# Kernel optimization log

Measured on AMD Instinct MI355X. Metric: run time of the kernel, lower is better.

## Reference

```python
import jax, jax.numpy as jnp
import numpy as np

N, D_IN, UNITS = 8192, 4096, 4096

def setup_inputs() -> dict:
    key = jax.random.key(0)
    k1, k2 = jax.random.split(key)
    x = jax.random.normal(k1, (N, D_IN), dtype=jnp.float32)
    # weight initialized RandomNormal(stddev=0.1) in the original build()
    w = jax.random.normal(k2, (D_IN, UNITS), dtype=jnp.float32) * 0.1
    return {"x": x, "w": w}

def reference(x, w):
    # BinaryDense: sign-binarize both activations and weights, then dense matmul.
    # tf.sign semantics: sign(0) == 0, matched by jnp.sign.
    x_bin = jnp.sign(x)  # [N, d_in]
    w_bin = jnp.sign(w)  # [d_in, units]
    return jnp.matmul(x_bin, w_bin)  # [N, units]
```

## Files before the change

### kernel.cpp

```cpp
#include <hip/hip_runtime.h>
#include <stdint.h>

#define M_DIM 8192
#define K_DIM 4096
#define N_DIM 4096
#define KB (K_DIM / 2)

typedef unsigned char u8;
typedef unsigned int u32;
typedef int i32x4 __attribute__((ext_vector_type(4)));
typedef int i32x8 __attribute__((ext_vector_type(8)));
typedef float f32x4 __attribute__((ext_vector_type(4)));
typedef float float4v __attribute__((ext_vector_type(4)));
typedef u32 u32x2 __attribute__((ext_vector_type(2)));

__device__ __forceinline__ u32 sign_fp4(float v) {
  return v > 0.0f ? 0x2u : (v < 0.0f ? 0xAu : 0x0u);
}

__device__ __forceinline__ u32 pk16(u32 v) {
  return (v & 0xFu) | ((v >> 4) & 0xF0u) | ((v >> 8) & 0xF00u) | ((v >> 12) & 0xF000u);
}

__global__ void binarize_fused(const float* __restrict__ x, const float* __restrict__ w,
                               u32* __restrict__ xb, u8* __restrict__ wT) {
  const int tid = threadIdx.x;
  if (blockIdx.x < 4096) {
    __shared__ u8 tile[64][68];
    const int bid = blockIdx.x;
    const int bn = (bid & 63) * 64;
    const int bk = (bid >> 6) * 64;

#pragma unroll
    for (int it = 0; it < 4; ++it) {
      int idx = tid + it * 256;
      int r = idx >> 4;
      int c = (idx & 15) * 4;
      float4v v = *(const float4v*)&w[(size_t)(bk + r) * N_DIM + bn + c];
      tile[c + 0][r] = (u8)sign_fp4(v.x);
      tile[c + 1][r] = (u8)sign_fp4(v.y);
      tile[c + 2][r] = (u8)sign_fp4(v.z);
      tile[c + 3][r] = (u8)sign_fp4(v.w);
    }
    __syncthreads();
    const int rn = tid >> 2;
    const int cbyte = (tid & 3) * 8;
    const u32* trow = (const u32*)&tile[rn][0];
    u32 q0 = trow[cbyte / 2 + 0];
    u32 q1 = trow[cbyte / 2 + 1];
    u32 q2 = trow[cbyte / 2 + 2];
    u32 q3 = trow[cbyte / 2 + 3];
    u32x2 o;
    o.x = pk16(q0) | (pk16(q1) << 16);
    o.y = pk16(q2) | (pk16(q3) << 16);
    *(u32x2*)&wT[(size_t)(bn + rn) * KB + (bk >> 1) + cbyte] = o;
  } else {
    const int n8 = M_DIM * K_DIM / 8;
    int i = (blockIdx.x - 4096) * 256 + tid;
    const int stride = 2048 * 256;
    for (; i < n8; i += stride) {
      float4v v0 = ((const float4v*)x)[2 * i];
      float4v v1 = ((const float4v*)x)[2 * i + 1];
      u32 wd = sign_fp4(v0.x) | (sign_fp4(v0.y) << 4) | (sign_fp4(v0.z) << 8) |
               (sign_fp4(v0.w) << 12) | (sign_fp4(v1.x) << 16) | (sign_fp4(v1.y) << 20) |
               (sign_fp4(v1.z) << 24) | (sign_fp4(v1.w) << 28);
      xb[i] = wd;
    }
  }
}

#define BM 256
#define BN 256
#define BKB 128
#define NT (K_DIM / 256)

__device__ __forceinline__ void gload_lds16(const u8* g, u8* l) {
  __builtin_amdgcn_global_load_lds(
      (const __attribute__((address_space(1))) void*)g,
      (__attribute__((address_space(3))) void*)l, 16, 0, 0);
}

__device__ __forceinline__ i32x8 pad8(i32x4 v) {
  return __builtin_shufflevector(v, v, 0, 1, 2, 3, -1, -1, -1, -1);
}

__device__ __forceinline__ f32x4 mfma_fp4(i32x4 a, i32x4 b, f32x4 c) {
  return __builtin_amdgcn_mfma_scale_f32_16x16x128_f8f6f4(pad8(a), pad8(b), c, 4, 4, 0, 0x7F, 0,
                                                          0x7F);
}

__global__ __launch_bounds__(512, 2) void gemm_bin_fp4(const u8* __restrict__ A,
                                                       const u8* __restrict__ Bt,
                                                       float* __restrict__ C) {
  __shared__ u8 lds[2][4][128 * 128];

  const int tid = threadIdx.x;
  const int lane = tid & 63;
  const int wid = tid >> 6;
  const int wr = wid >> 2;
  const int wc = wid & 3;

  const int b = blockIdx.x;
  const int sw = (b & 7) * (gridDim.x >> 3) + (b >> 3);
  const int tiles_n = N_DIM / BN;
  const int bm = (sw / tiles_n) * BM;
  const int bn = (sw % tiles_n) * BN;

  const int l15 = lane & 15;
  const int g4 = lane >> 4;
  const int srow = lane >> 3;
  const int swz_src = (((lane & 7) ^ srow) << 4);

  auto stage = [&](int buf, int slot, const u8* gbase) {
#pragma unroll
    for (int i = 0; i < 2; ++i) {
      const u8* g = gbase + (size_t)(i * 64 + wid * 8 + srow) * KB + swz_src;
      gload_lds16(g, &lds[buf][slot][(i * 64 + wid * 8) * 128]);
    }
  };

  f32x4 acc[8][4] = {};

  {
    const u8* Abase = A + (size_t)bm * KB;
    const u8* Bbase = Bt + (size_t)bn * KB;
    stage(0, 0, Abase);
    stage(0, 1, Abase + (size_t)128 * KB);
    stage(0, 2, Bbase);
    stage(0, 3, Bbase + (size_t)128 * KB);
    stage(1, 2, Bbase + BKB);
    stage(1, 3, Bbase + (size_t)128 * KB + BKB);
  }
  asm volatile("s_waitcnt vmcnt(4)" ::: "memory");
  __builtin_amdgcn_s_barrier();

  i32x4 av[4], b0[4], b1[4];

  for (int t = 0; t < NT; ++t) {
    const int buf = t & 1;
    const u8* As = &lds[buf][wr][0];
    const u8* Bs = &lds[buf][2 + (wc >> 1)][0];
    const int brow0 = (wc & 1) * 64;
    const u8* Anext = A + (size_t)bm * KB + (t + 1) * BKB;
    const u8* Bnext2 = Bt + (size_t)bn * KB + (t + 2) * BKB;

#pragma unroll
    for (int m = 0; m < 4; ++m) {
      int row = m * 16 + l15;
      int col = (g4 * 16) ^ ((row & 7) << 4);
      av[m] = *(const i32x4*)&As[row * 128 + col];
    }
#pragma unroll
    for (int n = 0; n < 4; ++n) {
      int row = brow0 + n * 16 + l15;
      int col = (g4 * 16) ^ ((row & 7) << 4);
      b0[n] = *(const i32x4*)&Bs[row * 128 + col];
    }
    if (t + 1 < NT) stage(buf ^ 1, 0, Anext);
    __builtin_amdgcn_s_barrier();
    asm volatile("s_waitcnt lgkmcnt(0)" ::: "memory");
    __builtin_amdgcn_sched_barrier(0);
    __builtin_amdgcn_s_setprio(1);
#pragma unroll
    for (int m = 0; m < 4; ++m)
#pragma unroll
      for (int n = 0; n < 4; ++n)
        acc[m][n] = mfma_fp4(av[m], b0[n], acc[m][n]);
    __builtin_amdgcn_s_setprio(0);
    __builtin_amdgcn_s_barrier();

#pragma unroll
    for (int m = 0; m < 4; ++m) {
      int row = m * 16 + l15;
      int col = (64 + g4 * 16) ^ ((row & 7) << 4);
      av[m] = *(const i32x4*)&As[row * 128 + col];
    }
#pragma unroll
    for (int n = 0; n < 4; ++n) {
      int row = brow0 + n * 16 + l15;
      int col = (64 + g4 * 16) ^ ((row & 7) << 4);
      b1[n] = *(const i32x4*)&Bs[row * 128 + col];
    }
    if (t + 1 < NT) stage(buf ^ 1, 1, Anext + (size_t)128 * KB);
    __builtin_amdgcn_s_barrier();
    asm volatile("s_waitcnt lgkmcnt(0)" ::: "memory");
    __builtin_amdgcn_sched_barrier(0);
    __builtin_amdgcn_s_setprio(1);
#pragma unroll
    for (int m = 0; m < 4; ++m)
#pragma unroll
      for (int n = 0; n < 4; ++n)
        acc[m][n] = mfma_fp4(av[m], b1[n], acc[m][n]);
    __builtin_amdgcn_s_setprio(0);
    __builtin_amdgcn_s_barrier();

#pragma unroll
    for (int m = 0; m < 4; ++m) {
      int row = 64 + m * 16 + l15;
      int col = (g4 * 16) ^ ((row & 7) << 4);
      av[m] = *(const i32x4*)&As[row * 128 + col];
    }
    if (t + 2 < NT) stage(buf, 2, Bnext2);
    __builtin_amdgcn_s_barrier();
    asm volatile("s_waitcnt lgkmcnt(0)" ::: "memory");
    __builtin_amdgcn_sched_barrier(0);
    __builtin_amdgcn_s_setprio(1);
#pragma unroll
    for (int m = 0; m < 4; ++m)
#pragma unroll
      for (int n = 0; n < 4; ++n)
        acc[4 + m][n] = mfma_fp4(av[m], b0[n], acc[4 + m][n]);
    __builtin_amdgcn_s_setprio(0);
    __builtin_amdgcn_s_barrier();

#pragma unroll
    for (int m = 0; m < 4; ++m) {
      int row = 64 + m * 16 + l15;
      int col = (64 + g4 * 16) ^ ((row & 7) << 4);
      av[m] = *(const i32x4*)&As[row * 128 + col];
    }
    if (t + 2 < NT) stage(buf, 3, Bnext2 + (size_t)128 * KB);
    __builtin_amdgcn_s_barrier();
    asm volatile("s_waitcnt lgkmcnt(0)" ::: "memory");
    __builtin_amdgcn_sched_barrier(0);
    __builtin_amdgcn_s_setprio(1);
#pragma unroll
    for (int m = 0; m < 4; ++m)
#pragma unroll
      for (int n = 0; n < 4; ++n)
        acc[4 + m][n] = mfma_fp4(av[m], b1[n], acc[4 + m][n]);
    __builtin_amdgcn_s_setprio(0);
    if (t + 2 < NT)
      asm volatile("s_waitcnt vmcnt(4)" ::: "memory");
    else
      asm volatile("s_waitcnt vmcnt(0)" ::: "memory");
    __builtin_amdgcn_s_barrier();
  }

  const int crow0 = bm + wr * 128;
  const int ccol0 = bn + wc * 64;
#pragma unroll
  for (int m = 0; m < 8; ++m)
#pragma unroll
    for (int n = 0; n < 4; ++n)
#pragma unroll
      for (int j = 0; j < 4; ++j)
        C[(size_t)(crow0 + m * 16 + g4 * 4 + j) * N_DIM + ccol0 + n * 16 + l15] = acc[m][n][j];
}

__global__ void naive_bin_gemm(const float* __restrict__ X, const float* __restrict__ W,
                               float* __restrict__ C) {
  int j = blockIdx.x * blockDim.x + threadIdx.x;
  int i = blockIdx.y;
  if (j >= N_DIM) return;
  float s = 0.0f;
  for (int k = 0; k < K_DIM; ++k) {
    float xv = X[(size_t)i * K_DIM + k];
    float wv = W[(size_t)k * N_DIM + j];
    float sx = (float)((xv > 0.0f) - (xv < 0.0f));
    float sw = (float)((wv > 0.0f) - (wv < 0.0f));
    s += sx * sw;
  }
  C[(size_t)i * N_DIM + j] = s;
}

extern "C" void kernel_launch(void* const* d_in, const int* in_sizes, int n_in,
                              void* d_out, int out_size, void* d_ws, size_t ws_size,
                              hipStream_t stream) {
  const float* x = (const float*)d_in[0];
  const float* w = (const float*)d_in[1];
  float* out = (float*)d_out;

  const size_t xb_bytes = (size_t)M_DIM * KB;
  const size_t wt_bytes = (size_t)N_DIM * KB;

  if (ws_size >= xb_bytes + wt_bytes) {
    u8* xb = (u8*)d_ws;
    u8* wt = (u8*)((char*)d_ws + xb_bytes);

    binarize_fused<<<4096 + 2048, 256, 0, stream>>>(x, w, (u32*)xb, wt);

    const int grid = (M_DIM / BM) * (N_DIM / BN);
    gemm_bin_fp4<<<grid, 512, 0, stream>>>(xb, wt, out);
  } else {
    naive_bin_gemm<<<dim3(N_DIM / 256, M_DIM), dim3(256), 0, stream>>>(x, w, out);
  }
}
```

Baseline: 127.4 us.

## Interleave binarize block roles and cut GEMM barriers by loading all fragments upfront

The binarize kernel now interleaves weight-transpose blocks and activation-pack blocks (two weight tiles, then one x block, repeating) so both kinds of memory traffic are in flight together instead of one finishing after the other. The GEMM main loop loads all A and B fragments for a k-step into separate registers up front. It issues both global-to-LDS stages together and drops most of the per-phase s_barrier and lgkmcnt waits, leaving one barrier before the B prefetch. This is meant to cut synchronisation stalls and let LDS reads overlap MFMA work. The cost is higher register pressure, and relying on compiler-inserted waits may raise LDS hazard risk if the stage ordering is subtly wrong.

```diff
diff --git a/kernel.cpp b/kernel.cpp
--- a/kernel.cpp
+++ b/kernel.cpp
@@ -25,22 +25,24 @@
 __global__ void binarize_fused(const float* __restrict__ x, const float* __restrict__ w,
                                u32* __restrict__ xb, u8* __restrict__ wT) {
   const int tid = threadIdx.x;
-  if (blockIdx.x < 4096) {
+  const int bid = blockIdx.x;
+  const int r3 = bid % 3;
+  if (r3 != 2) {
     __shared__ u8 tile[64][68];
-    const int bid = blockIdx.x;
-    const int bn = (bid & 63) * 64;
-    const int bk = (bid >> 6) * 64;
+    const int wtile = (bid / 3) * 2 + r3;
+    const int bn = (wtile & 63) * 64;
+    const int bk = (wtile >> 6) * 64;
 
 #pragma unroll
     for (int it = 0; it < 4; ++it) {
       int idx = tid + it * 256;
-      int r = idx >> 4;
+      int rr = idx >> 4;
       int c = (idx & 15) * 4;
-      float4v v = *(const float4v*)&w[(size_t)(bk + r) * N_DIM + bn + c];
-      tile[c + 0][r] = (u8)sign_fp4(v.x);
-      tile[c + 1][r] = (u8)sign_fp4(v.y);
-      tile[c + 2][r] = (u8)sign_fp4(v.z);
-      tile[c + 3][r] = (u8)sign_fp4(v.w);
+      float4v v = *(const float4v*)&w[(size_t)(bk + rr) * N_DIM + bn + c];
+      tile[c + 0][rr] = (u8)sign_fp4(v.x);
+      tile[c + 1][rr] = (u8)sign_fp4(v.y);
+      tile[c + 2][rr] = (u8)sign_fp4(v.z);
+      tile[c + 3][rr] = (u8)sign_fp4(v.w);
     }
     __syncthreads();
     const int rn = tid >> 2;
@@ -56,7 +58,7 @@
     *(u32x2*)&wT[(size_t)(bn + rn) * KB + (bk >> 1) + cbyte] = o;
   } else {
     const int n8 = M_DIM * K_DIM / 8;
-    int i = (blockIdx.x - 4096) * 256 + tid;
+    int i = (bid / 3) * 256 + tid;
     const int stride = 2048 * 256;
     for (; i < n8; i += stride) {
       float4v v0 = ((const float4v*)x)[2 * i];
@@ -134,8 +136,6 @@
   asm volatile("s_waitcnt vmcnt(4)" ::: "memory");
   __builtin_amdgcn_s_barrier();
 
-  i32x4 av[4], b0[4], b1[4];
-
   for (int t = 0; t < NT; ++t) {
     const int buf = t & 1;
     const u8* As = &lds[buf][wr][0];
@@ -144,11 +144,13 @@
     const u8* Anext = A + (size_t)bm * KB + (t + 1) * BKB;
     const u8* Bnext2 = Bt + (size_t)bn * KB + (t + 2) * BKB;
 
+    i32x4 a0[4], a1[4], a2[4], a3[4], b0[4], b1[4];
+
 #pragma unroll
     for (int m = 0; m < 4; ++m) {
       int row = m * 16 + l15;
       int col = (g4 * 16) ^ ((row & 7) << 4);
-      av[m] = *(const i32x4*)&As[row * 128 + col];
+      a0[m] = *(const i32x4*)&As[row * 128 + col];
     }
 #pragma unroll
     for (int n = 0; n < 4; ++n) {
@@ -156,24 +158,17 @@
       int col = (g4 * 16) ^ ((row & 7) << 4);
       b0[n] = *(const i32x4*)&Bs[row * 128 + col];
     }
-    if (t + 1 < NT) stage(buf ^ 1, 0, Anext);
-    __builtin_amdgcn_s_barrier();
-    asm volatile("s_waitcnt lgkmcnt(0)" ::: "memory");
-    __builtin_amdgcn_sched_barrier(0);
-    __builtin_amdgcn_s_setprio(1);
-#pragma unroll
-    for (int m = 0; m < 4; ++m)
-#pragma unroll
-      for (int n = 0; n < 4; ++n)
-        acc[m][n] = mfma_fp4(av[m], b0[n], acc[m][n]);
-    __builtin_amdgcn_s_setprio(0);
-    __builtin_amdgcn_s_barrier();
+    if (t + 1 < NT) {
+      stage(buf ^ 1, 0, Anext);
+      stage(buf ^ 1, 1, Anext + (size_t)128 * KB);
+    }
+    __builtin_amdgcn_sched_barrier(0);
 
 #pragma unroll
     for (int m = 0; m < 4; ++m) {
       int row = m * 16 + l15;
       int col = (64 + g4 * 16) ^ ((row & 7) << 4);
-      av[m] = *(const i32x4*)&As[row * 128 + col];
+      a1[m] = *(const i32x4*)&As[row * 128 + col];
     }
 #pragma unroll
     for (int n = 0; n < 4; ++n) {
@@ -181,55 +176,64 @@
       int col = (64 + g4 * 16) ^ ((row & 7) << 4);
       b1[n] = *(const i32x4*)&Bs[row * 128 + col];
     }
-    if (t + 1 < NT) stage(buf ^ 1, 1, Anext + (size_t)128 * KB);
-    __builtin_amdgcn_s_barrier();
-    asm volatile("s_waitcnt lgkmcnt(0)" ::: "memory");
-    __builtin_amdgcn_sched_barrier(0);
-    __builtin_amdgcn_s_setprio(1);
-#pragma unroll
-    for (int m = 0; m < 4; ++m)
-#pragma unroll
-      for (int n = 0; n < 4; ++n)
-        acc[m][n] = mfma_fp4(av[m], b1[n], acc[m][n]);
-    __builtin_amdgcn_s_setprio(0);
-    __builtin_amdgcn_s_barrier();
+    __builtin_amdgcn_sched_barrier(0);
+
+    __builtin_amdgcn_s_setprio(1);
+#pragma unroll
+    for (int m = 0; m < 4; ++m)
+#pragma unroll
+      for (int n = 0; n < 4; ++n)
+        acc[m][n] = mfma_fp4(a0[m], b0[n], acc[m][n]);
+    __builtin_amdgcn_s_setprio(0);
+    __builtin_amdgcn_sched_barrier(0);
 
 #pragma unroll
     for (int m = 0; m < 4; ++m) {
       int row = 64 + m * 16 + l15;
       int col = (g4 * 16) ^ ((row & 7) << 4);
-      av[m] = *(const i32x4*)&As[row * 128 + col];
-    }
-    if (t + 2 < NT) stage(buf, 2, Bnext2);
-    __builtin_amdgcn_s_barrier();
-    asm volatile("s_waitcnt lgkmcnt(0)" ::: "memory");
-    __builtin_amdgcn_sched_barrier(0);
-    __builtin_amdgcn_s_setprio(1);
-#pragma unroll
-    for (int m = 0; m < 4; ++m)
-#pragma unroll
-      for (int n = 0; n < 4; ++n)
-        acc[4 + m][n] = mfma_fp4(av[m], b0[n], acc[4 + m][n]);
-    __builtin_amdgcn_s_setprio(0);
-    __builtin_amdgcn_s_barrier();
-
+      a2[m] = *(const i32x4*)&As[row * 128 + col];
+    }
 #pragma unroll
     for (int m = 0; m < 4; ++m) {
       int row = 64 + m * 16 + l15;
       int col = (64 + g4 * 16) ^ ((row & 7) << 4);
-      av[m] = *(const i32x4*)&As[row * 128 + col];
-    }
-    if (t + 2 < NT) stage(buf, 3, Bnext2 + (size_t)128 * KB);
+      a3[m] = *(const i32x4*)&As[row * 128 + col];
+    }
+    __builtin_amdgcn_sched_barrier(0);
+
+    __builtin_amdgcn_s_setprio(1);
+#pragma unroll
+    for (int m = 0; m < 4; ++m)
+#pragma unroll
+      for (int n = 0; n < 4; ++n)
+        acc[m][n] = mfma_fp4(a1[m], b1[n], acc[m][n]);
+    __builtin_amdgcn_s_setprio(0);
+
     __builtin_amdgcn_s_barrier();
-    asm volatile("s_waitcnt lgkmcnt(0)" ::: "memory");
-    __builtin_amdgcn_sched_barrier(0);
-    __builtin_amdgcn_s_setprio(1);
-#pragma unroll
-    for (int m = 0; m < 4; ++m)
-#pragma unroll
-      for (int n = 0; n < 4; ++n)
-        acc[4 + m][n] = mfma_fp4(av[m], b1[n], acc[4 + m][n]);
-    __builtin_amdgcn_s_setprio(0);
+
+    if (t + 2 < NT) {
+      stage(buf, 2, Bnext2);
+      stage(buf, 3, Bnext2 + (size_t)128 * KB);
+    }
+    __builtin_amdgcn_sched_barrier(0);
+
+    __builtin_amdgcn_s_setprio(1);
+#pragma unroll
+    for (int m = 0; m < 4; ++m)
+#pragma unroll
+      for (int n = 0; n < 4; ++n)
+        acc[4 + m][n] = mfma_fp4(a2[m], b0[n], acc[4 + m][n]);
+    __builtin_amdgcn_s_setprio(0);
+    __builtin_amdgcn_sched_barrier(0);
+
+    __builtin_amdgcn_s_setprio(1);
+#pragma unroll
+    for (int m = 0; m < 4; ++m)
+#pragma unroll
+      for (int n = 0; n < 4; ++n)
+        acc[4 + m][n] = mfma_fp4(a3[m], b1[n], acc[4 + m][n]);
+    __builtin_amdgcn_s_setprio(0);
+
     if (t + 2 < NT)
       asm volatile("s_waitcnt vmcnt(4)" ::: "memory");
     else
@@ -278,7 +282,7 @@
     u8* xb = (u8*)d_ws;
     u8* wt = (u8*)((char*)d_ws + xb_bytes);
 
-    binarize_fused<<<4096 + 2048, 256, 0, stream>>>(x, w, (u32*)xb, wt);
+    binarize_fused<<<6144, 256, 0, stream>>>(x, w, (u32*)xb, wt);
 
     const int grid = (M_DIM / BM) * (N_DIM / BN);
     gemm_bin_fp4<<<grid, 512, 0, stream>>>(xb, wt, out);
```

Result: no change. 125.8 us (-1.3%).
